# Optimization experiments

Measured on AMD Instinct MI355X. Metric: run time of the kernel, lower is better.

Reference implementation:

```python
import jax, jax.numpy as jnp
import numpy as np

E, H, F, K = 8, 1024, 4096, 2  # experts, hidden, intermediate, top-k
B, S = 4, 2048


def setup_inputs() -> dict:
    key = jax.random.key(0)
    ks = jax.random.split(key, 6)
    x = jax.random.normal(ks[0], (B, S, H), dtype=jnp.float32)
    gate_w = jax.random.normal(ks[1], (H, E), dtype=jnp.float32) * 0.02
    gate_b = jnp.zeros((E,), dtype=jnp.float32)
    Wg = jax.random.normal(ks[2], (E, H, F), dtype=jnp.float32) * 0.02
    Wu = jax.random.normal(ks[3], (E, H, F), dtype=jnp.float32) * 0.02
    Wd = jax.random.normal(ks[4], (E, F, H), dtype=jnp.float32) * 0.02
    return {"x": x, "gate_w": gate_w, "gate_b": gate_b, "Wg": Wg, "Wu": Wu, "Wd": Wd}


def _moe_forward(x, gate_w, gate_b, Wg, Wu, Wd):
    xf = x.reshape(-1, x.shape[-1])                      # [T, H]
    T = xf.shape[0]
    logits = xf @ gate_w + gate_b                        # [T, E]  (gate_logit)
    top_vals, top_idx = jax.lax.top_k(logits, K)         # [T, K]
    # scatter top-k logits into -inf background, softmax -> zero weight for unselected experts
    sparse = jnp.full_like(logits, -jnp.inf)
    sparse = sparse.at[jnp.arange(T)[:, None], top_idx].set(top_vals)
    gate_weights = jax.nn.softmax(sparse, axis=-1)       # [T, E], exactly 0 off top-k

    # sum_e w_e * Expert_e(x); scan over the small expert axis to bound memory
    def expert_step(acc, params):
        wg, wu, wd, w = params                           # wg:[H,F] wu:[H,F] wd:[F,H] w:[T]
        h = jax.nn.silu(xf @ wg) * (xf @ wu)             # [T, F]
        y = h @ wd                                       # [T, H]
        return acc + w[:, None] * y, None

    acc0 = jnp.zeros_like(xf)
    acc, _ = jax.lax.scan(expert_step, acc0, (Wg, Wu, Wd, gate_weights.T))
    return acc.reshape(x.shape), logits


def reference(x, gate_w, gate_b, Wg, Wu, Wd):
    return _moe_forward(x, gate_w, gate_b, Wg, Wu, Wd)
```

## Files before the change

### kernel.cpp

```cpp
#include <hip/hip_runtime.h>
#include <cstdint>

#define TTOK 8192
#define HID  1024
#define FFD  4096
#define NEXP 8
#define NASSIGN 16384
#define MAXMB 24

typedef __attribute__((ext_vector_type(8))) short bf16x8;
typedef __attribute__((ext_vector_type(4))) float f32x4;

__device__ __forceinline__ unsigned short f2bf(float f) {
  unsigned int u = __builtin_bit_cast(unsigned int, f);
  u += 0x7FFFu + ((u >> 16) & 1u);
  return (unsigned short)(u >> 16);
}

__device__ __forceinline__ float bf2f(unsigned short s) {
  unsigned int u = (unsigned int)s << 16;
  return __builtin_bit_cast(float, u);
}

__device__ __forceinline__ void gload16(const unsigned short* g, unsigned short* l) {
  __builtin_amdgcn_global_load_lds(
      (const __attribute__((address_space(1))) unsigned int*)g,
      (__attribute__((address_space(3))) unsigned int*)l, 16, 0, 0);
}


__global__ void zero_counts_kernel(int* counts) {
  if (threadIdx.x < NEXP) counts[threadIdx.x] = 0;
}

__global__ void gate_kernel(const float* __restrict__ x,
                            const float* __restrict__ gw,
                            const float* __restrict__ gb,
                            float* __restrict__ logits_out,
                            int* __restrict__ counts,
                            int* __restrict__ te, int* __restrict__ tp,
                            float* __restrict__ tw) {
  const int lane = threadIdx.x & 63;
  const int wib  = threadIdx.x >> 6;
  const int t = blockIdx.x * 4 + wib;
  const float* xr = x + (size_t)t * HID;

  float acc[NEXP];
#pragma unroll
  for (int e = 0; e < NEXP; ++e) acc[e] = 0.f;

#pragma unroll
  for (int i = 0; i < HID / 64; ++i) {
    int h = lane + 64 * i;
    float xv = xr[h];
    const float* g = gw + h * NEXP;
#pragma unroll
    for (int e = 0; e < NEXP; ++e) acc[e] += xv * g[e];
  }
#pragma unroll
  for (int off = 32; off; off >>= 1)
#pragma unroll
    for (int e = 0; e < NEXP; ++e) acc[e] += __shfl_xor(acc[e], off);
#pragma unroll
  for (int e = 0; e < NEXP; ++e) acc[e] += gb[e];

  if (lane < NEXP) logits_out[(size_t)t * NEXP + lane] = acc[lane];

  if (lane == 0) {
    int e0 = 0; float v0 = acc[0];
#pragma unroll
    for (int e = 1; e < NEXP; ++e) if (acc[e] > v0) { v0 = acc[e]; e0 = e; }
    int e1 = -1; float v1 = -3.4e38f;
#pragma unroll
    for (int e = 0; e < NEXP; ++e) if (e != e0 && acc[e] > v1) { v1 = acc[e]; e1 = e; }
    float s = __expf(v1 - v0);
    float w0 = 1.f / (1.f + s);
    float w1 = s * w0;
    int p0 = atomicAdd(&counts[e0], 1);
    int p1 = atomicAdd(&counts[e1], 1);
    te[t * 2] = e0; te[t * 2 + 1] = e1;
    tp[t * 2] = p0; tp[t * 2 + 1] = p1;
    tw[t * 2] = w0; tw[t * 2 + 1] = w1;
  }
}

__global__ void scatter_kernel(const int* __restrict__ counts, int* __restrict__ offsets,
                               const int* __restrict__ te, const int* __restrict__ tp,
                               const float* __restrict__ tw,
                               int* __restrict__ tok_of, float* __restrict__ wt_of,
                               int* __restrict__ asn_of) {
  __shared__ int offs[NEXP];
  if (threadIdx.x == 0) {
    int run = 0;
    for (int e = 0; e < NEXP; ++e) { offs[e] = run; offsets[e] = run; run += counts[e]; }
  }
  __syncthreads();
  for (int t = threadIdx.x; t < TTOK; t += blockDim.x) {
#pragma unroll
    for (int j = 0; j < 2; ++j) {
      int e = te[t * 2 + j];
      int a = offs[e] + tp[t * 2 + j];
      tok_of[a] = t;
      wt_of[a] = tw[t * 2 + j];
      asn_of[t * 2 + j] = a;
    }
  }
}


__global__ void convert_x_kernel(const float* __restrict__ x, unsigned short* __restrict__ xb) {
  size_t i = ((size_t)blockIdx.x * 256 + threadIdx.x) * 8;
  float4 a = *(const float4*)(x + i);
  float4 b = *(const float4*)(x + i + 4);
  union { unsigned short us[8]; uint4 v; } u;
  u.us[0] = f2bf(a.x); u.us[1] = f2bf(a.y); u.us[2] = f2bf(a.z); u.us[3] = f2bf(a.w);
  u.us[4] = f2bf(b.x); u.us[5] = f2bf(b.y); u.us[6] = f2bf(b.z); u.us[7] = f2bf(b.w);
  *(uint4*)(xb + i) = u.v;
}

__global__ void transpose_cvt_kernel(const float* __restrict__ src,
                                     unsigned short* __restrict__ dst, int R, int C) {
  __shared__ float tile[64][65];
  const int r0 = blockIdx.y * 64, c0 = blockIdx.x * 64;
  const size_t base = (size_t)blockIdx.z * (size_t)R * C;
  src += base; dst += base;
  const int tid = threadIdx.x;
  {
    const int c4 = (tid & 15) * 4, rr = tid >> 4;
#pragma unroll
    for (int i = 0; i < 4; ++i) {
      int row = rr + i * 16;
      float4 v = *(const float4*)&src[(size_t)(r0 + row) * C + c0 + c4];
      tile[row][c4 + 0] = v.x; tile[row][c4 + 1] = v.y;
      tile[row][c4 + 2] = v.z; tile[row][c4 + 3] = v.w;
    }
  }
  __syncthreads();
  {
    const int r4 = (tid & 15) * 4, cc = tid >> 4;
#pragma unroll
    for (int i = 0; i < 4; ++i) {
      int c = cc + i * 16;
      ushort4 o;
      o.x = f2bf(tile[r4 + 0][c]);
      o.y = f2bf(tile[r4 + 1][c]);
      o.z = f2bf(tile[r4 + 2][c]);
      o.w = f2bf(tile[r4 + 3][c]);
      *(ushort4*)&dst[(size_t)(c0 + c) * R + r0 + r4] = o;
    }
  }
}


__global__ __launch_bounds__(256, 2) void moe_up_kernel(
    const unsigned short* __restrict__ xb,
    const unsigned short* __restrict__ WgT,
    const unsigned short* __restrict__ WuT,
    const int* __restrict__ counts, const int* __restrict__ offsets,
    const int* __restrict__ tok_of,
    unsigned short* __restrict__ hbuf)
{
  const int e = blockIdx.x & 7;
  const int mblk = blockIdx.x >> 3;
  const int cnt = counts[e];
  if (mblk * 128 >= cnt) return;
  const int off = offsets[e];
  const int n0 = blockIdx.y * 128;

  __shared__ __align__(16) unsigned short As[2][128 * 32];
  __shared__ __align__(16) unsigned short Bgs[2][128 * 32];
  __shared__ __align__(16) unsigned short Bus[2][128 * 32];
  __shared__ int toks[128];

  const int tid = threadIdx.x;
  const int lane = tid & 63;
  const int w = tid >> 6;

  if (tid < 128) {
    int a = off + mblk * 128 + tid;
    if (a > NASSIGN - 1) a = NASSIGN - 1;
    toks[tid] = tok_of[a];
  }
  __syncthreads();

  const unsigned short* asrc[2];
  const unsigned short* bgsrc[2];
  const unsigned short* busrc[2];
#pragma unroll
  for (int j = 0; j < 2; ++j) {
    int rrow = w * 32 + j * 16 + (lane >> 2);
    int kcol = 8 * (lane & 3);
    asrc[j]  = xb  + (size_t)toks[rrow] * HID + kcol;
    bgsrc[j] = WgT + ((size_t)e * FFD + n0 + rrow) * HID + kcol;
    busrc[j] = WuT + ((size_t)e * FFD + n0 + rrow) * HID + kcol;
  }

  auto STAGE = [&](int buf, int k0) {
#pragma unroll
    for (int j = 0; j < 2; ++j) {
      gload16(asrc[j]  + k0, &As[buf][w * 1024 + j * 512]);
      gload16(bgsrc[j] + k0, &Bgs[buf][w * 1024 + j * 512]);
      gload16(busrc[j] + k0, &Bus[buf][w * 1024 + j * 512]);
    }
  };

  f32x4 accg[4][4] = {};
  f32x4 accu[4][4] = {};
  const int wr = (w >> 1) * 64, wc = (w & 1) * 64;
  const int lr = lane & 15, kg = (lane >> 4) * 8;

  STAGE(0, 0);
#pragma unroll 1
  for (int t = 0; t < HID / 32; ++t) {
    const int cur = t & 1;
    if (t + 1 < HID / 32) {
      STAGE(cur ^ 1, (t + 1) * 32);
      asm volatile("s_waitcnt vmcnt(6)" ::: "memory");
    } else {
      asm volatile("s_waitcnt vmcnt(0)" ::: "memory");
    }
    __builtin_amdgcn_s_barrier();

    bf16x8 af[4], bgf[4], buf_[4];
#pragma unroll
    for (int m = 0; m < 4; ++m)
      af[m] = *(const bf16x8*)&As[cur][(wr + m * 16 + lr) * 32 + kg];
#pragma unroll
    for (int n = 0; n < 4; ++n) {
      bgf[n]  = *(const bf16x8*)&Bgs[cur][(wc + n * 16 + lr) * 32 + kg];
      buf_[n] = *(const bf16x8*)&Bus[cur][(wc + n * 16 + lr) * 32 + kg];
    }
#pragma unroll
    for (int m = 0; m < 4; ++m)
#pragma unroll
      for (int n = 0; n < 4; ++n) {
        accg[m][n] = __builtin_amdgcn_mfma_f32_16x16x32_bf16(af[m], bgf[n],  accg[m][n], 0, 0, 0);
        accu[m][n] = __builtin_amdgcn_mfma_f32_16x16x32_bf16(af[m], buf_[n], accu[m][n], 0, 0, 0);
      }
    __builtin_amdgcn_s_barrier();
  }

  const int crb = (lane >> 4) * 4, cc = lane & 15;
#pragma unroll
  for (int m = 0; m < 4; ++m)
#pragma unroll
    for (int n = 0; n < 4; ++n)
#pragma unroll
      for (int r = 0; r < 4; ++r) {
        int lrow = wr + m * 16 + crb + r;
        int grow = mblk * 128 + lrow;
        if (grow < cnt) {
          size_t a = (size_t)off + grow;
          float g = accg[m][n][r];
          float u = accu[m][n][r];
          float sg = g / (1.0f + __expf(-g));
          hbuf[a * FFD + (n0 + wc + n * 16 + cc)] = f2bf(sg * u);
        }
      }
}

__global__ __launch_bounds__(256, 2) void moe_down_kernel(
    const unsigned short* __restrict__ hb,
    const unsigned short* __restrict__ WdT,
    const int* __restrict__ counts, const int* __restrict__ offsets,
    unsigned short* __restrict__ ypart)
{
  const int e = blockIdx.x & 7;
  const int mblk = blockIdx.x >> 3;
  const int cnt = counts[e];
  if (mblk * 128 >= cnt) return;
  const int off = offsets[e];
  const int n0 = blockIdx.y * 128;

  __shared__ __align__(16) unsigned short As[2][128 * 32];
  __shared__ __align__(16) unsigned short Bs[2][128 * 32];

  const int tid = threadIdx.x;
  const int lane = tid & 63;
  const int w = tid >> 6;

  const unsigned short* asrc[2];
  const unsigned short* bsrc[2];
#pragma unroll
  for (int j = 0; j < 2; ++j) {
    int rrow = w * 32 + j * 16 + (lane >> 2);
    int kcol = 8 * (lane & 3);
    int a = off + mblk * 128 + rrow;
    if (a > NASSIGN - 1) a = NASSIGN - 1;
    asrc[j] = hb + (size_t)a * FFD + kcol;
    bsrc[j] = WdT + ((size_t)e * HID + n0 + rrow) * FFD + kcol;
  }

  auto STAGE = [&](int buf, int k0) {
#pragma unroll
    for (int j = 0; j < 2; ++j) {
      gload16(asrc[j] + k0, &As[buf][w * 1024 + j * 512]);
      gload16(bsrc[j] + k0, &Bs[buf][w * 1024 + j * 512]);
    }
  };

  f32x4 acc[4][4] = {};
  const int wr = (w >> 1) * 64, wc = (w & 1) * 64;
  const int lr = lane & 15, kg = (lane >> 4) * 8;

  STAGE(0, 0);
#pragma unroll 1
  for (int t = 0; t < FFD / 32; ++t) {
    const int cur = t & 1;
    if (t + 1 < FFD / 32) {
      STAGE(cur ^ 1, (t + 1) * 32);
      asm volatile("s_waitcnt vmcnt(4)" ::: "memory");
    } else {
      asm volatile("s_waitcnt vmcnt(0)" ::: "memory");
    }
    __builtin_amdgcn_s_barrier();

    bf16x8 af[4], bf_[4];
#pragma unroll
    for (int m = 0; m < 4; ++m)
      af[m] = *(const bf16x8*)&As[cur][(wr + m * 16 + lr) * 32 + kg];
#pragma unroll
    for (int n = 0; n < 4; ++n)
      bf_[n] = *(const bf16x8*)&Bs[cur][(wc + n * 16 + lr) * 32 + kg];
#pragma unroll
    for (int m = 0; m < 4; ++m)
#pragma unroll
      for (int n = 0; n < 4; ++n)
        acc[m][n] = __builtin_amdgcn_mfma_f32_16x16x32_bf16(af[m], bf_[n], acc[m][n], 0, 0, 0);
    __builtin_amdgcn_s_barrier();
  }

  const int crb = (lane >> 4) * 4, cc = lane & 15;
#pragma unroll
  for (int m = 0; m < 4; ++m)
#pragma unroll
    for (int n = 0; n < 4; ++n)
#pragma unroll
      for (int r = 0; r < 4; ++r) {
        int lrow = wr + m * 16 + crb + r;
        int grow = mblk * 128 + lrow;
        if (grow < cnt)
          ypart[((size_t)off + grow) * HID + (n0 + wc + n * 16 + cc)] = f2bf(acc[m][n][r]);
      }
}

__global__ void combine_kernel(const unsigned short* __restrict__ ypart,
                               const int* __restrict__ asn_of,
                               const float* __restrict__ wt_of,
                               float* __restrict__ y) {
  const int t = blockIdx.x;
  const int a0 = asn_of[t * 2], a1 = asn_of[t * 2 + 1];
  const float w0 = wt_of[a0], w1 = wt_of[a1];
  const int c = threadIdx.x * 4;
  ushort4 p0 = *(const ushort4*)&ypart[(size_t)a0 * HID + c];
  ushort4 p1 = *(const ushort4*)&ypart[(size_t)a1 * HID + c];
  float4 r;
  r.x = w0 * bf2f(p0.x) + w1 * bf2f(p1.x);
  r.y = w0 * bf2f(p0.y) + w1 * bf2f(p1.y);
  r.z = w0 * bf2f(p0.z) + w1 * bf2f(p1.z);
  r.w = w0 * bf2f(p0.w) + w1 * bf2f(p1.w);
  *(float4*)&y[(size_t)t * HID + c] = r;
}


extern "C" void kernel_launch(void* const* d_in, const int* in_sizes, int n_in,
                              void* d_out, int out_size, void* d_ws, size_t ws_size,
                              hipStream_t stream) {
  const float* x  = (const float*)d_in[0];
  const float* gw = (const float*)d_in[1];
  const float* gb = (const float*)d_in[2];
  const float* Wg = (const float*)d_in[3];
  const float* Wu = (const float*)d_in[4];
  const float* Wd = (const float*)d_in[5];
  float* out = (float*)d_out;
  float* logits = out + (size_t)TTOK * HID;

  char* ws = (char*)d_ws;
  size_t o = 0;
  auto carve = [&](size_t b) { char* p = ws + o; o += (b + 255) & ~(size_t)255; return p; };
  int*   counts  = (int*)carve(NEXP * 4);
  int*   offsets = (int*)carve(NEXP * 4);
  int*   te      = (int*)carve((size_t)TTOK * 2 * 4);
  int*   tp      = (int*)carve((size_t)TTOK * 2 * 4);
  float* tw      = (float*)carve((size_t)TTOK * 2 * 4);
  int*   tok_of  = (int*)carve((size_t)NASSIGN * 4);
  float* wt_of   = (float*)carve((size_t)NASSIGN * 4);
  int*   asn_of  = (int*)carve((size_t)TTOK * 2 * 4);
  unsigned short* xb  = (unsigned short*)carve((size_t)TTOK * HID * 2);
  unsigned short* WgT = (unsigned short*)carve((size_t)NEXP * FFD * HID * 2);
  unsigned short* WuT = (unsigned short*)carve((size_t)NEXP * FFD * HID * 2);
  unsigned short* WdT = (unsigned short*)carve((size_t)NEXP * HID * FFD * 2);
  unsigned short* hb  = (unsigned short*)carve((size_t)NASSIGN * FFD * 2);
  unsigned short* ypart = (unsigned short*)carve((size_t)NASSIGN * HID * 2);
  (void)ws_size; (void)in_sizes; (void)n_in; (void)out_size;

  zero_counts_kernel<<<dim3(1), dim3(64), 0, stream>>>(counts);
  gate_kernel<<<dim3(TTOK / 4), dim3(256), 0, stream>>>(x, gw, gb, logits, counts, te, tp, tw);
  scatter_kernel<<<dim3(1), dim3(256), 0, stream>>>(counts, offsets, te, tp, tw, tok_of, wt_of, asn_of);
  convert_x_kernel<<<dim3((TTOK * HID) / 2048), dim3(256), 0, stream>>>(x, xb);
  transpose_cvt_kernel<<<dim3(FFD / 64, HID / 64, NEXP), dim3(256), 0, stream>>>(Wg, WgT, HID, FFD);
  transpose_cvt_kernel<<<dim3(FFD / 64, HID / 64, NEXP), dim3(256), 0, stream>>>(Wu, WuT, HID, FFD);
  transpose_cvt_kernel<<<dim3(HID / 64, FFD / 64, NEXP), dim3(256), 0, stream>>>(Wd, WdT, FFD, HID);
  moe_up_kernel<<<dim3(NEXP * MAXMB, FFD / 128), dim3(256), 0, stream>>>(xb, WgT, WuT, counts, offsets, tok_of, hb);
  moe_down_kernel<<<dim3(NEXP * MAXMB, HID / 128), dim3(256), 0, stream>>>(hb, WdT, counts, offsets, ypart);
  combine_kernel<<<dim3(TTOK), dim3(256), 0, stream>>>(ypart, asn_of, wt_of, out);
}
```

Measured before the change: 970.7 us.

## Rework expert GEMMs into 256-row tiles with 4-stage swizzled LDS pipeline

Both expert GEMM kernels move to 512-thread blocks covering 256 token rows, with a single 4-deep LDS ring buffer. Global-to-LDS loads are issued three K-steps ahead, and the LDS layout is XOR-swizzled to cut bank conflicts. Each K-step is split into two half-tiles so the next stage's A and B loads interleave with MFMA work, and MFMA sections are wrapped in s_setprio. This aims to raise data reuse per block and hide load latency, at the cost of 128KB of LDS, one block per CU, and more barriers per iteration.

```diff
diff --git a/kernel.cpp b/kernel.cpp
--- a/kernel.cpp
+++ b/kernel.cpp
@@ -6,7 +6,7 @@
 #define FFD  4096
 #define NEXP 8
 #define NASSIGN 16384
-#define MAXMB 24
+#define MCAP 12
 
 typedef __attribute__((ext_vector_type(8))) short bf16x8;
 typedef __attribute__((ext_vector_type(4))) float f32x4;
@@ -152,7 +152,8 @@
 }
 
 
-__global__ __launch_bounds__(256, 2) void moe_up_kernel(
+
+__global__ __launch_bounds__(512, 1) void moe_up_kernel(
     const unsigned short* __restrict__ xb,
     const unsigned short* __restrict__ WgT,
     const unsigned short* __restrict__ WuT,
@@ -163,103 +164,122 @@
   const int e = blockIdx.x & 7;
   const int mblk = blockIdx.x >> 3;
   const int cnt = counts[e];
-  if (mblk * 128 >= cnt) return;
+  if (mblk * 256 >= cnt) return;
   const int off = offsets[e];
   const int n0 = blockIdx.y * 128;
 
-  __shared__ __align__(16) unsigned short As[2][128 * 32];
-  __shared__ __align__(16) unsigned short Bgs[2][128 * 32];
-  __shared__ __align__(16) unsigned short Bus[2][128 * 32];
-  __shared__ int toks[128];
+  __shared__ __align__(16) unsigned short L[4][16384];
+  __shared__ int toks[256];
 
   const int tid = threadIdx.x;
   const int lane = tid & 63;
   const int w = tid >> 6;
 
-  if (tid < 128) {
-    int a = off + mblk * 128 + tid;
+  for (int i = tid; i < 256; i += 512) {
+    int a = off + mblk * 256 + i;
     if (a > NASSIGN - 1) a = NASSIGN - 1;
-    toks[tid] = tok_of[a];
+    toks[i] = tok_of[a];
   }
   __syncthreads();
 
-  const unsigned short* asrc[2];
-  const unsigned short* bgsrc[2];
-  const unsigned short* busrc[2];
-#pragma unroll
-  for (int j = 0; j < 2; ++j) {
-    int rrow = w * 32 + j * 16 + (lane >> 2);
-    int kcol = 8 * (lane & 3);
-    asrc[j]  = xb  + (size_t)toks[rrow] * HID + kcol;
-    bgsrc[j] = WgT + ((size_t)e * FFD + n0 + rrow) * HID + kcol;
-    busrc[j] = WuT + ((size_t)e * FFD + n0 + rrow) * HID + kcol;
-  }
-
-  auto STAGE = [&](int buf, int k0) {
-#pragma unroll
-    for (int j = 0; j < 2; ++j) {
-      gload16(asrc[j]  + k0, &As[buf][w * 1024 + j * 512]);
-      gload16(bgsrc[j] + k0, &Bgs[buf][w * 1024 + j * 512]);
-      gload16(busrc[j] + k0, &Bus[buf][w * 1024 + j * 512]);
+  const int sr = tid >> 2, st = tid & 3;
+  const int scol = ((st ^ ((sr >> 2) & 3)) << 3);
+  const unsigned short* a0p = xb + (size_t)toks[sr] * HID + scol;
+  const unsigned short* a1p = xb + (size_t)toks[128 + sr] * HID + scol;
+  const unsigned short* bgp = WgT + ((size_t)e * FFD + n0 + sr) * HID + scol;
+  const unsigned short* bup = WuT + ((size_t)e * FFD + n0 + sr) * HID + scol;
+
+  auto SP0 = [&](int g) {
+    unsigned short* H = &L[g & 3][0];
+    gload16(a0p + g * 32, H + tid * 8);
+    gload16(a1p + g * 32, H + 4096 + tid * 8);
+  };
+  auto SP1 = [&](int g) {
+    unsigned short* H = &L[g & 3][0];
+    gload16(bgp + g * 32, H + 8192 + tid * 8);
+    gload16(bup + g * 32, H + 12288 + tid * 8);
+  };
+
+  const int lr = lane & 15, lq = lane >> 4;
+  const int rdswz = ((lq ^ ((lr >> 2) & 3)) << 3);
+  const int wm = w >> 2, wn = w & 3;
+
+  f32x4 accg[8][2] = {};
+  f32x4 accu[8][2] = {};
+
+  SP0(0); SP1(0); SP0(1); SP1(1); SP0(2); SP1(2);
+
+  const int NH = HID / 32;
+  bf16x8 bg[2], bu[2];
+#pragma unroll 4
+  for (int g = 0; g < NH; ++g) {
+    const unsigned short* H = &L[g & 3][0];
+    const int rem = NH - 1 - g;
+    if (rem >= 2)      asm volatile("s_waitcnt vmcnt(8)" ::: "memory");
+    else if (rem == 1) asm volatile("s_waitcnt vmcnt(4)" ::: "memory");
+    else               asm volatile("s_waitcnt vmcnt(0)" ::: "memory");
+    __builtin_amdgcn_s_barrier();
+
+    bf16x8 af[4];
+#pragma unroll
+    for (int m = 0; m < 4; ++m)
+      af[m] = *(const bf16x8*)(H + (wm * 128 + m * 16 + lr) * 32 + rdswz);
+#pragma unroll
+    for (int nn = 0; nn < 2; ++nn) {
+      bg[nn] = *(const bf16x8*)(H + 8192  + (wn * 32 + nn * 16 + lr) * 32 + rdswz);
+      bu[nn] = *(const bf16x8*)(H + 12288 + (wn * 32 + nn * 16 + lr) * 32 + rdswz);
     }
-  };
-
-  f32x4 accg[4][4] = {};
-  f32x4 accu[4][4] = {};
-  const int wr = (w >> 1) * 64, wc = (w & 1) * 64;
-  const int lr = lane & 15, kg = (lane >> 4) * 8;
-
-  STAGE(0, 0);
-#pragma unroll 1
-  for (int t = 0; t < HID / 32; ++t) {
-    const int cur = t & 1;
-    if (t + 1 < HID / 32) {
-      STAGE(cur ^ 1, (t + 1) * 32);
-      asm volatile("s_waitcnt vmcnt(6)" ::: "memory");
-    } else {
-      asm volatile("s_waitcnt vmcnt(0)" ::: "memory");
-    }
-    __builtin_amdgcn_s_barrier();
-
-    bf16x8 af[4], bgf[4], buf_[4];
-#pragma unroll
-    for (int m = 0; m < 4; ++m)
-      af[m] = *(const bf16x8*)&As[cur][(wr + m * 16 + lr) * 32 + kg];
-#pragma unroll
-    for (int n = 0; n < 4; ++n) {
-      bgf[n]  = *(const bf16x8*)&Bgs[cur][(wc + n * 16 + lr) * 32 + kg];
-      buf_[n] = *(const bf16x8*)&Bus[cur][(wc + n * 16 + lr) * 32 + kg];
-    }
-#pragma unroll
-    for (int m = 0; m < 4; ++m)
-#pragma unroll
-      for (int n = 0; n < 4; ++n) {
-        accg[m][n] = __builtin_amdgcn_mfma_f32_16x16x32_bf16(af[m], bgf[n],  accg[m][n], 0, 0, 0);
-        accu[m][n] = __builtin_amdgcn_mfma_f32_16x16x32_bf16(af[m], buf_[n], accu[m][n], 0, 0, 0);
+    if (g + 3 < NH) SP0(g + 3);
+    asm volatile("s_waitcnt lgkmcnt(0)" ::: "memory");
+    __builtin_amdgcn_s_setprio(1);
+#pragma unroll
+    for (int m = 0; m < 4; ++m)
+#pragma unroll
+      for (int nn = 0; nn < 2; ++nn) {
+        accg[m][nn] = __builtin_amdgcn_mfma_f32_16x16x32_bf16(af[m], bg[nn], accg[m][nn], 0, 0, 0);
+        accu[m][nn] = __builtin_amdgcn_mfma_f32_16x16x32_bf16(af[m], bu[nn], accu[m][nn], 0, 0, 0);
       }
-    __builtin_amdgcn_s_barrier();
+    __builtin_amdgcn_s_setprio(0);
+    __builtin_amdgcn_s_barrier();
+
+#pragma unroll
+    for (int m = 0; m < 4; ++m)
+      af[m] = *(const bf16x8*)(H + (wm * 128 + 64 + m * 16 + lr) * 32 + rdswz);
+    if (g + 3 < NH) SP1(g + 3);
+    __builtin_amdgcn_s_barrier();
+    asm volatile("s_waitcnt lgkmcnt(0)" ::: "memory");
+    __builtin_amdgcn_s_setprio(1);
+#pragma unroll
+    for (int m = 0; m < 4; ++m)
+#pragma unroll
+      for (int nn = 0; nn < 2; ++nn) {
+        accg[4 + m][nn] = __builtin_amdgcn_mfma_f32_16x16x32_bf16(af[m], bg[nn], accg[4 + m][nn], 0, 0, 0);
+        accu[4 + m][nn] = __builtin_amdgcn_mfma_f32_16x16x32_bf16(af[m], bu[nn], accu[4 + m][nn], 0, 0, 0);
+      }
+    __builtin_amdgcn_s_setprio(0);
   }
 
   const int crb = (lane >> 4) * 4, cc = lane & 15;
 #pragma unroll
-  for (int m = 0; m < 4; ++m)
-#pragma unroll
-    for (int n = 0; n < 4; ++n)
+  for (int m = 0; m < 8; ++m)
+#pragma unroll
+    for (int nn = 0; nn < 2; ++nn)
 #pragma unroll
       for (int r = 0; r < 4; ++r) {
-        int lrow = wr + m * 16 + crb + r;
-        int grow = mblk * 128 + lrow;
+        int lrow = wm * 128 + (m >> 2) * 64 + (m & 3) * 16 + crb + r;
+        int grow = mblk * 256 + lrow;
         if (grow < cnt) {
           size_t a = (size_t)off + grow;
-          float g = accg[m][n][r];
-          float u = accu[m][n][r];
+          float g = accg[m][nn][r];
+          float u = accu[m][nn][r];
           float sg = g / (1.0f + __expf(-g));
-          hbuf[a * FFD + (n0 + wc + n * 16 + cc)] = f2bf(sg * u);
+          hbuf[a * FFD + (n0 + wn * 32 + nn * 16 + cc)] = f2bf(sg * u);
         }
       }
 }
 
-__global__ __launch_bounds__(256, 2) void moe_down_kernel(
+
+__global__ __launch_bounds__(512, 1) void moe_down_kernel(
     const unsigned short* __restrict__ hb,
     const unsigned short* __restrict__ WdT,
     const int* __restrict__ counts, const int* __restrict__ offsets,
@@ -268,79 +288,99 @@
   const int e = blockIdx.x & 7;
   const int mblk = blockIdx.x >> 3;
   const int cnt = counts[e];
-  if (mblk * 128 >= cnt) return;
+  if (mblk * 256 >= cnt) return;
   const int off = offsets[e];
-  const int n0 = blockIdx.y * 128;
-
-  __shared__ __align__(16) unsigned short As[2][128 * 32];
-  __shared__ __align__(16) unsigned short Bs[2][128 * 32];
+  const int n0 = blockIdx.y * 256;
+
+  __shared__ __align__(16) unsigned short L[4][16384];
 
   const int tid = threadIdx.x;
   const int lane = tid & 63;
   const int w = tid >> 6;
 
-  const unsigned short* asrc[2];
-  const unsigned short* bsrc[2];
-#pragma unroll
-  for (int j = 0; j < 2; ++j) {
-    int rrow = w * 32 + j * 16 + (lane >> 2);
-    int kcol = 8 * (lane & 3);
-    int a = off + mblk * 128 + rrow;
-    if (a > NASSIGN - 1) a = NASSIGN - 1;
-    asrc[j] = hb + (size_t)a * FFD + kcol;
-    bsrc[j] = WdT + ((size_t)e * HID + n0 + rrow) * FFD + kcol;
-  }
-
-  auto STAGE = [&](int buf, int k0) {
-#pragma unroll
-    for (int j = 0; j < 2; ++j) {
-      gload16(asrc[j] + k0, &As[buf][w * 1024 + j * 512]);
-      gload16(bsrc[j] + k0, &Bs[buf][w * 1024 + j * 512]);
-    }
+  const int sr = tid >> 2, st = tid & 3;
+  const int scol = ((st ^ ((sr >> 2) & 3)) << 3);
+  int ar0 = off + mblk * 256 + sr;       if (ar0 > NASSIGN - 1) ar0 = NASSIGN - 1;
+  int ar1 = off + mblk * 256 + 128 + sr; if (ar1 > NASSIGN - 1) ar1 = NASSIGN - 1;
+  const unsigned short* a0p = hb + (size_t)ar0 * FFD + scol;
+  const unsigned short* a1p = hb + (size_t)ar1 * FFD + scol;
+  const unsigned short* b0p = WdT + ((size_t)e * HID + n0 + sr) * FFD + scol;
+  const unsigned short* b1p = WdT + ((size_t)e * HID + n0 + 128 + sr) * FFD + scol;
+
+  auto SP0 = [&](int g) {
+    unsigned short* H = &L[g & 3][0];
+    gload16(a0p + g * 32, H + tid * 8);
+    gload16(a1p + g * 32, H + 4096 + tid * 8);
   };
-
-  f32x4 acc[4][4] = {};
-  const int wr = (w >> 1) * 64, wc = (w & 1) * 64;
-  const int lr = lane & 15, kg = (lane >> 4) * 8;
-
-  STAGE(0, 0);
-#pragma unroll 1
-  for (int t = 0; t < FFD / 32; ++t) {
-    const int cur = t & 1;
-    if (t + 1 < FFD / 32) {
-      STAGE(cur ^ 1, (t + 1) * 32);
-      asm volatile("s_waitcnt vmcnt(4)" ::: "memory");
-    } else {
-      asm volatile("s_waitcnt vmcnt(0)" ::: "memory");
-    }
-    __builtin_amdgcn_s_barrier();
-
-    bf16x8 af[4], bf_[4];
-#pragma unroll
-    for (int m = 0; m < 4; ++m)
-      af[m] = *(const bf16x8*)&As[cur][(wr + m * 16 + lr) * 32 + kg];
+  auto SP1 = [&](int g) {
+    unsigned short* H = &L[g & 3][0];
+    gload16(b0p + g * 32, H + 8192 + tid * 8);
+    gload16(b1p + g * 32, H + 12288 + tid * 8);
+  };
+
+  const int lr = lane & 15, lq = lane >> 4;
+  const int rdswz = ((lq ^ ((lr >> 2) & 3)) << 3);
+  const int wm = w >> 2, wn = w & 3;
+
+  f32x4 acc[8][4] = {};
+
+  SP0(0); SP1(0); SP0(1); SP1(1); SP0(2); SP1(2);
+
+  const int NH = FFD / 32;
+  bf16x8 bf_[4];
+#pragma unroll 4
+  for (int g = 0; g < NH; ++g) {
+    const unsigned short* H = &L[g & 3][0];
+    const int rem = NH - 1 - g;
+    if (rem >= 2)      asm volatile("s_waitcnt vmcnt(8)" ::: "memory");
+    else if (rem == 1) asm volatile("s_waitcnt vmcnt(4)" ::: "memory");
+    else               asm volatile("s_waitcnt vmcnt(0)" ::: "memory");
+    __builtin_amdgcn_s_barrier();
+
+    bf16x8 af[4];
+#pragma unroll
+    for (int m = 0; m < 4; ++m)
+      af[m] = *(const bf16x8*)(H + (wm * 128 + m * 16 + lr) * 32 + rdswz);
 #pragma unroll
     for (int n = 0; n < 4; ++n)
-      bf_[n] = *(const bf16x8*)&Bs[cur][(wc + n * 16 + lr) * 32 + kg];
+      bf_[n] = *(const bf16x8*)(H + 8192 + (wn * 64 + n * 16 + lr) * 32 + rdswz);
+    if (g + 3 < NH) SP0(g + 3);
+    asm volatile("s_waitcnt lgkmcnt(0)" ::: "memory");
+    __builtin_amdgcn_s_setprio(1);
 #pragma unroll
     for (int m = 0; m < 4; ++m)
 #pragma unroll
       for (int n = 0; n < 4; ++n)
         acc[m][n] = __builtin_amdgcn_mfma_f32_16x16x32_bf16(af[m], bf_[n], acc[m][n], 0, 0, 0);
-    __builtin_amdgcn_s_barrier();
+    __builtin_amdgcn_s_setprio(0);
+    __builtin_amdgcn_s_barrier();
+
+#pragma unroll
+    for (int m = 0; m < 4; ++m)
+      af[m] = *(const bf16x8*)(H + (wm * 128 + 64 + m * 16 + lr) * 32 + rdswz);
+    if (g + 3 < NH) SP1(g + 3);
+    __builtin_amdgcn_s_barrier();
+    asm volatile("s_waitcnt lgkmcnt(0)" ::: "memory");
+    __builtin_amdgcn_s_setprio(1);
+#pragma unroll
+    for (int m = 0; m < 4; ++m)
+#pragma unroll
+      for (int n = 0; n < 4; ++n)
+        acc[4 + m][n] = __builtin_amdgcn_mfma_f32_16x16x32_bf16(af[m], bf_[n], acc[4 + m][n], 0, 0, 0);
+    __builtin_amdgcn_s_setprio(0);
   }
 
   const int crb = (lane >> 4) * 4, cc = lane & 15;
 #pragma unroll
-  for (int m = 0; m < 4; ++m)
+  for (int m = 0; m < 8; ++m)
 #pragma unroll
     for (int n = 0; n < 4; ++n)
 #pragma unroll
       for (int r = 0; r < 4; ++r) {
-        int lrow = wr + m * 16 + crb + r;
-        int grow = mblk * 128 + lrow;
+        int lrow = wm * 128 + (m >> 2) * 64 + (m & 3) * 16 + crb + r;
+        int grow = mblk * 256 + lrow;
         if (grow < cnt)
-          ypart[((size_t)off + grow) * HID + (n0 + wc + n * 16 + cc)] = f2bf(acc[m][n][r]);
+          ypart[((size_t)off + grow) * HID + (n0 + wn * 64 + n * 16 + cc)] = f2bf(acc[m][n][r]);
       }
 }
 
@@ -401,7 +441,7 @@
   transpose_cvt_kernel<<<dim3(FFD / 64, HID / 64, NEXP), dim3(256), 0, stream>>>(Wg, WgT, HID, FFD);
   transpose_cvt_kernel<<<dim3(FFD / 64, HID / 64, NEXP), dim3(256), 0, stream>>>(Wu, WuT, HID, FFD);
   transpose_cvt_kernel<<<dim3(HID / 64, FFD / 64, NEXP), dim3(256), 0, stream>>>(Wd, WdT, FFD, HID);
-  moe_up_kernel<<<dim3(NEXP * MAXMB, FFD / 128), dim3(256), 0, stream>>>(xb, WgT, WuT, counts, offsets, tok_of, hb);
-  moe_down_kernel<<<dim3(NEXP * MAXMB, HID / 128), dim3(256), 0, stream>>>(hb, WdT, counts, offsets, ypart);
+  moe_up_kernel<<<dim3(NEXP * MCAP, FFD / 128), dim3(512), 0, stream>>>(xb, WgT, WuT, counts, offsets, tok_of, hb);
+  moe_down_kernel<<<dim3(NEXP * MCAP, HID / 256), dim3(512), 0, stream>>>(hb, WdT, counts, offsets, ypart);
   combine_kernel<<<dim3(TTOK), dim3(256), 0, stream>>>(ypart, asn_of, wt_of, out);
 }
```

New measurement: 999.4 us. 1.03x slower.
